# Kernel optimization log

Hardware: AMD Instinct MI355X
Metric: run time of the kernel (lower is better)

The kernel has to match this reference:

```python
import jax, jax.numpy as jnp
import numpy as np

B, T, C, H, W = 2, 8, 4, 128, 128
P = 8; D = 128; DEPTH = 2; E = 4; HD = 2 * D
Hp, Wp = H // P, W // P; F2 = 2 * D; CPP = C * P * P


def _ln(x, g, b):
    m = x.mean(-1, keepdims=True)
    v = ((x - m) ** 2).mean(-1, keepdims=True)
    return (x - m) * jax.lax.rsqrt(v + 1e-5) * g + b


def setup_inputs():
    key = jax.random.key(0)
    it = iter(jax.random.split(key, 32))
    def n(shape, s=0.02):
        return jax.random.normal(next(it), shape, jnp.float32) * s
    z = lambda shape: jnp.zeros(shape, jnp.float32)
    return {
        "x": jax.random.normal(next(it), (B, T, C, H, W), jnp.float32),
        "dt": jax.random.uniform(next(it), (T,), jnp.float32, 0.1, 1.0),
        "enc_Wre": n((CPP, D)), "enc_Wim": n((CPP, D)),
        "dec_W": n((F2, CPP)), "dec_b": z((CPP,)),
        "ln_sp_g": jnp.ones((DEPTH, F2), jnp.float32), "ln_sp_b": z((DEPTH, F2)),
        "conv_W": n((DEPTH, F2, F2, 3, 3), 0.05), "conv_b": z((DEPTH, F2)),
        "E_re": n((DEPTH, D, D), 0.05), "E_im": n((DEPTH, D, D), 0.05),
        "Dc_re": n((DEPTH, D, D), 0.05), "Dc_im": n((DEPTH, D, D), 0.05),
        "gate_W": n((DEPTH, F2, D)), "gate_b": z((DEPTH, D)),
        "src_W": n((DEPTH, F2, F2)), "src_b": z((DEPTH, F2)),
        "flux_decay": z((DEPTH, D)),
        "lam_re": n((DEPTH, D), 0.5), "lam_im": n((DEPTH, D), 0.5),
        "ln_t_g": jnp.ones((DEPTH, F2), jnp.float32), "ln_t_b": z((DEPTH, F2)),
        "rtr_W": n((DEPTH, F2, E)),
        "W1": n((DEPTH, E, F2, HD)), "b1": z((DEPTH, E, HD)),
        "W2": n((DEPTH, E, HD, F2)), "b2": z((DEPTH, E, F2)),
    }


def _forward(x, dt, enc_Wre, enc_Wim, dec_W, dec_b, ln_sp_g, ln_sp_b, conv_W, conv_b,
             E_re, E_im, Dc_re, Dc_im, gate_W, gate_b, src_W, src_b, flux_decay,
             lam_re, lam_im, ln_t_g, ln_t_b, rtr_W, W1, b1, W2, b2):
    Bx, Tx = x.shape[:2]
    # patch-embed encoder -> complex latent [B,T,D,Hp,Wp]
    f = x.reshape(Bx, Tx, C, Hp, P, Wp, P).transpose(0, 1, 3, 5, 2, 4, 6).reshape(Bx, Tx, Hp, Wp, CPP)
    zc = (f @ enc_Wre) + 1j * (f @ enc_Wim)
    zc = zc.transpose(0, 1, 4, 2, 3)
    dtBT = jnp.broadcast_to(dt[None, :], (Bx, Tx))
    flux = jnp.zeros((Bx, D), jnp.complex64)
    for i in range(DEPTH):
        # spatial branch: LayerNorm over [re,im] channels + Clifford-style 3x3 conv
        zr = jnp.concatenate([zc.real, zc.imag], axis=2).reshape(Bx * Tx, F2, Hp, Wp)
        xn = _ln(zr.transpose(0, 2, 3, 1), ln_sp_g[i], ln_sp_b[i]).transpose(0, 3, 1, 2)
        xs = jax.lax.conv_general_dilated(xn, conv_W[i], (1, 1), 'SAME',
                                          dimension_numbers=('NCHW', 'OIHW', 'NCHW')) + conv_b[i][None, :, None, None]
        sre, sim = jnp.split(xs, 2, axis=1)
        zc = zc + (sre + 1j * sim).reshape(Bx, Tx, D, Hp, Wp)
        # eigen-basis encode (complex channel mixing)
        xe = zc.transpose(0, 1, 3, 4, 2) @ (E_re[i] + 1j * E_im[i])  # B,T,Hp,Wp,D
        xm = xe.mean(axis=(2, 3))  # B,T,D complex
        # sequential flux tracker: inherently recurrent -> lax.scan over T
        gW, gb, sW, sb = gate_W[i], gate_b[i], src_W[i], src_b[i]
        dec = jax.nn.sigmoid(flux_decay[i])
        def step(fl, xmt):
            inp = jnp.concatenate([xmt.real, xmt.imag], -1)
            gate = jax.nn.sigmoid(inp @ gW + gb)
            s2 = inp @ sW + sb
            src = s2[..., :D] + 1j * s2[..., D:]
            fn = dec * fl + gate * xmt + (1.0 - gate) * src
            return fn, (fn, src)
        flux, (flux_seq, src_seq) = jax.lax.scan(step, flux, xm.transpose(1, 0, 2))
        flux_seq = flux_seq.transpose(1, 0, 2)
        src_seq = src_seq.transpose(1, 0, 2)
        g = jax.nn.sigmoid(jnp.concatenate([flux_seq.real, flux_seq.imag], -1) @ gW + gb)[:, :, None, None, :]
        forcing = xe * g + src_seq[:, :, None, None, :] * (1.0 - g)
        # complex transition operators (ZOH-style discretization)
        lam = -jax.nn.softplus(lam_re[i]) + 1j * lam_im[i]  # [D]
        opd = jnp.exp(dtBT[:, :, None] * lam[None, None, :])  # B,T,D complex
        opf = (opd - 1.0) / lam
        u = forcing * opf[:, :, None, None, :]
        A = jnp.broadcast_to(opd[:, :, None, None, :], u.shape)
        def comb(a, b):
            aA, aX = a
            bA, bX = b
            return (aA * bA, bX + bA * aX)
        # parallel pscan over time: h_t = A_t*h_{t-1} + u_t, independent per (B,Hp,Wp)
        _, uo = jax.lax.associative_scan(comb, (A, u), axis=1)
        xo = uo @ (Dc_re[i] + 1j * Dc_im[i])  # basis decode, B,T,Hp,Wp,D
        xon = _ln(jnp.concatenate([xo.real, xo.imag], -1), ln_t_g[i], ln_t_b[i])
        xcc = xon[..., :D] + 1j * xon[..., D:]
        # MoE FFN with soft routing over experts
        ft = jnp.concatenate([xcc.real, xcc.imag], -1).reshape(-1, F2)  # [M,2D]
        gates = jax.nn.softmax(ft @ rtr_W[i], axis=-1)  # [M,E]
        hmid = jax.nn.gelu(jnp.einsum('mf,efh->emh', ft, W1[i]) + b1[i][:, None, :])
        oexp = jnp.einsum('emh,ehf->emf', hmid, W2[i]) + b2[i][:, None, :]
        dtok = jnp.einsum('me,emf->mf', gates, oexp).reshape(Bx, Tx, Hp, Wp, F2)
        delta = dtok[..., :D] + 1j * dtok[..., D:]
        zc = zc + (xcc + delta).transpose(0, 1, 4, 2, 3)
    # decoder: project [re,im] -> pixels and unpatchify (real output)
    zl = zc.transpose(0, 1, 3, 4, 2)
    fo = jnp.concatenate([zl.real, zl.imag], -1) @ dec_W + dec_b
    return fo.reshape(Bx, Tx, Hp, Wp, C, P, P).transpose(0, 1, 4, 2, 5, 3, 6).reshape(Bx, Tx, C, H, W)


def reference(x, dt, enc_Wre, enc_Wim, dec_W, dec_b, ln_sp_g, ln_sp_b, conv_W, conv_b,
              E_re, E_im, Dc_re, Dc_im, gate_W, gate_b, src_W, src_b, flux_decay,
              lam_re, lam_im, ln_t_g, ln_t_b, rtr_W, W1, b1, W2, b2):
    return _forward(x, dt, enc_Wre, enc_Wim, dec_W, dec_b, ln_sp_g, ln_sp_b, conv_W, conv_b,
                    E_re, E_im, Dc_re, Dc_im, gate_W, gate_b, src_W, src_b, flux_decay,
                    lam_re, lam_im, ln_t_g, ln_t_b, rtr_W, W1, b1, W2, b2)
```

## Files before the change

kernel.cpp:

```cpp
#include <hip/hip_runtime.h>
#include <hip/hip_bf16.h>
#include <math.h>


#define NIN 28
typedef unsigned short u16;
typedef __attribute__((ext_vector_type(8))) short bf16x8;
typedef __attribute__((ext_vector_type(4))) float f32x4;
typedef __attribute__((ext_vector_type(8))) unsigned short us8;
typedef __attribute__((ext_vector_type(4))) unsigned short us4;

__device__ __forceinline__ float b2f(u16 u){ union{unsigned i;float f;}v; v.i=((unsigned)u)<<16; return v.f; }
__device__ __forceinline__ u16 f2b(float x){ __hip_bfloat16 h=__float2bfloat16(x); return *(u16*)&h; }
__device__ __forceinline__ float loadraw(const void* p, size_t i, int bf){
  return bf? b2f(((const u16*)p)[i]) : ((const float*)p)[i];
}
__device__ __forceinline__ float d_sigmoid(float x){ return 1.0f/(1.0f+expf(-x)); }
__device__ __forceinline__ float d_softplus(float x){ return fmaxf(x,0.0f)+log1pf(expf(-fabsf(x))); }
__device__ __forceinline__ float d_gelu(float x){
  const float c=0.7978845608028654f;
  return 0.5f*x*(1.0f+tanhf(c*(x+0.044715f*x*x*x)));
}

__global__ void detect_k(const void* lnspg, int* flag){
  unsigned w=*(const unsigned*)lnspg;
  *flag=(w==0x3F803F80u)?1:0;
}

#define NF32 17
struct MP {
  const void* src[NIN];
  int f32dst[NF32]; int f32cum[NF32+1];
  int seg[7];
};

__global__ __launch_bounds__(256) void mega_prep(MP a, const int* __restrict__ flag, float* __restrict__ W,
    u16* __restrict__ encB, u16* __restrict__ decB, u16* __restrict__ convB,
    u16* __restrict__ cplxB, u16* __restrict__ w1B, u16* __restrict__ w2c){
  int g=blockIdx.x*256+threadIdx.x;
  if(g>=a.seg[6]) return;
  int bf=*flag;
  if(g<a.seg[0]){
    int i=0;
    while(i<NF32-1 && g>=a.f32cum[i+1]) i++;
    int local=g-a.f32cum[i];
    const int needs[NF32]={1,5,6,7,9,14,15,16,17,18,19,20,21,22,23,25,27};
    W[a.f32dst[i]+local]=loadraw(a.src[needs[i]], local, bf);
  } else if(g<a.seg[1]){
    int idx=g-a.seg[0]; int n=idx>>8, k=idx&255;
    float v=(n<128)? loadraw(a.src[2],(size_t)k*128+n,bf) : loadraw(a.src[3],(size_t)k*128+(n-128),bf);
    encB[idx]=f2b(v);
  } else if(g<a.seg[2]){
    int idx=g-a.seg[1]; int n=idx>>8, k=idx&255;
    decB[idx]=f2b(loadraw(a.src[4],(size_t)k*256+n,bf));
  } else if(g<a.seg[3]){
    int idx=g-a.seg[2];
    int i=idx/589824; int r=idx-i*589824;
    int o=r/2304; int k=r-o*2304;
    int kg=k>>8, ic=k&255; int ky=kg/3, kx=kg-3*ky;
    size_t s=((((size_t)i*256+o)*256+ic)*3+ky)*3+kx;
    convB[idx]=f2b(loadraw(a.src[8],s,bf));
  } else if(g<a.seg[4]){
    int idx=g-a.seg[3];
    int mat=idx>>16; int r=idx&65535; int n=r>>8, k=r&255;
    int depth=mat&1; int isD=mat>>1;
    const void* re=isD? a.src[12]:a.src[10];
    const void* im=isD? a.src[13]:a.src[11];
    size_t base=(size_t)depth*16384;
    float v;
    if(k<128){ v = (n<128)? loadraw(re,base+(size_t)k*128+n,bf) : loadraw(im,base+(size_t)k*128+(n-128),bf); }
    else{ int kk=k-128;
      v = (n<128)? -loadraw(im,base+(size_t)kk*128+n,bf) : loadraw(re,base+(size_t)kk*128+(n-128),bf); }
    cplxB[idx]=f2b(v);
  } else if(g<a.seg[5]){
    int idx=g-a.seg[4]; int m=idx>>16; int r=idx&65535; int n=r>>8, k=r&255;
    w1B[idx]=f2b(loadraw(a.src[24],(size_t)m*65536+(size_t)k*256+n,bf));
  } else {
    int idx=g-a.seg[5];
    int i=idx>>18; int r=idx&262143; int n=r>>10; int k=r&1023;
    int e=k>>8, h=k&255;
    size_t s=(((size_t)(i*4+e)*256+h)*256+n);
    w2c[idx]=f2b(loadraw(a.src[26],s,bf));
  }
}

#define FB_BIAS 1
#define FB_GELU 2
#define FB_RS 4
#define FB_ADDTO 8
#define FB_WF32 16
#define FB_WBF16 32
#define FB_CONV 64
#define FB_GATHER 128
#define FB_MOE2 256
#define FB_UNPATCH 512
#define FB_XM 1024

template<int FLAGS>
__global__ __launch_bounds__(256,4) void mfma_gemm(
    const void* __restrict__ Asrc, const u16* __restrict__ Bt,
    const float* __restrict__ bias, const float* __restrict__ gates,
    float* __restrict__ Cf, u16* __restrict__ Cb,
    const u16* __restrict__ Xtra, void* __restrict__ Cout, const int* __restrict__ flagp,
    int K, long aE, long bE, long biasE, long cE, long cRow,
    float* __restrict__ xm4)
{
  __shared__ u16 As[2][64][72];
  __shared__ u16 Bs[2][64][72];
  const int e=blockIdx.z;
  const u16* A=(const u16*)Asrc + (size_t)e*aE;
  Bt += (size_t)e*bE;
  const float* biasp = bias? bias+(size_t)e*biasE : nullptr;
  const int bn=blockIdx.x*64, bm=blockIdx.y*64;
  const int tid=threadIdx.x, l=tid&63, w=tid>>6;
  const int wm=w&1, wn=w>>1;
  int bf=0;
  if(FLAGS&(FB_GATHER|FB_UNPATCH)) bf=*flagp;
  const us8 z8={0,0,0,0,0,0,0,0};

  auto loadAi=[&](int k0, int i)->us8{
    int c=tid+(i<<8); int row=c>>3, col8=(c&7)<<3;
    int gk=k0+col8;
    if(FLAGS&FB_CONV){
      int m=bm+row; int bt=m>>8, rem=m&255, hp=rem>>4, wp=rem&15;
      int kg=gk>>8, ic=gk&255; int ky=kg/3, kx=kg-3*ky;
      int y=hp+ky-1, x=wp+kx-1;
      return ((unsigned)y<16u && (unsigned)x<16u)?
           *(const us8*)&A[(((size_t)(bt*16+y))*16+x)*256+ic] : z8;
    } else if(FLAGS&FB_GATHER){
      int m=bm+row; int bt=m>>8, rem=m&255, hp=rem>>4, wp=rem&15;
      int c2=gk>>6, ph=(gk>>3)&7;
      size_t sidx=(((size_t)bt*4+c2)<<14)+(size_t)((hp*8+ph)<<7)+wp*8;
      if(bf) return *(const us8*)&((const u16*)Asrc)[sidx];
      const float* xf=(const float*)Asrc + sidx;
      us8 t;
      #pragma unroll
      for(int j=0;j<8;j++) t[j]=f2b(xf[j]);
      return t;
    }
    return *(const us8*)&A[(size_t)(bm+row)*K+gk];
  };
  auto loadBi=[&](int k0, int i)->us8{
    int c=tid+(i<<8); int row=c>>3, col8=(c&7)<<3;
    return *(const us8*)&Bt[(size_t)(bn+row)*K+k0+col8];
  };

  us8 ra0,ra1,rb0,rb1;
  ra0=loadAi(0,0); ra1=loadAi(0,1); rb0=loadBi(0,0); rb1=loadBi(0,1);
  {
    int c0=tid, c1=tid+256;
    *(us8*)&As[0][c0>>3][(c0&7)<<3]=ra0;
    *(us8*)&As[0][c1>>3][(c1&7)<<3]=ra1;
    *(us8*)&Bs[0][c0>>3][(c0&7)<<3]=rb0;
    *(us8*)&Bs[0][c1>>3][(c1&7)<<3]=rb1;
  }
  const int kSteps=K>>6;
  if(kSteps>1){ ra0=loadAi(64,0); ra1=loadAi(64,1); rb0=loadBi(64,0); rb1=loadBi(64,1); }
  __syncthreads();

  f32x4 zf={0.f,0.f,0.f,0.f};
  f32x4 acc00=zf, acc01=zf, acc10=zf, acc11=zf;

  const int aRow0=wm*32+(l&15), bRow0=wn*32+(l&15);
  const int kcL=(l>>4)<<3;

  for(int ks=0; ks<kSteps; ++ks){
    const int cur=ks&1;
    if(ks+1<kSteps){
      int nb=cur^1;
      int c0=tid, c1=tid+256;
      *(us8*)&As[nb][c0>>3][(c0&7)<<3]=ra0;
      *(us8*)&As[nb][c1>>3][(c1&7)<<3]=ra1;
      *(us8*)&Bs[nb][c0>>3][(c0&7)<<3]=rb0;
      *(us8*)&Bs[nb][c1>>3][(c1&7)<<3]=rb1;
      if(ks+2<kSteps){
        int k0=(ks+2)<<6;
        ra0=loadAi(k0,0); ra1=loadAi(k0,1); rb0=loadBi(k0,0); rb1=loadBi(k0,1);
      }
    }
    #pragma unroll
    for(int kk=0;kk<64;kk+=32){
      const int kc=kk+kcL;
      bf16x8 a0=*(const bf16x8*)&As[cur][aRow0   ][kc];
      bf16x8 a1=*(const bf16x8*)&As[cur][aRow0+16][kc];
      bf16x8 b0=*(const bf16x8*)&Bs[cur][bRow0   ][kc];
      bf16x8 b1=*(const bf16x8*)&Bs[cur][bRow0+16][kc];
      acc00=__builtin_amdgcn_mfma_f32_16x16x32_bf16(a0,b0,acc00,0,0,0);
      acc01=__builtin_amdgcn_mfma_f32_16x16x32_bf16(a0,b1,acc01,0,0,0);
      acc10=__builtin_amdgcn_mfma_f32_16x16x32_bf16(a1,b0,acc10,0,0,0);
      acc11=__builtin_amdgcn_mfma_f32_16x16x32_bf16(a1,b1,acc11,0,0,0);
    }
    __syncthreads();
  }

  const int rr=(l>>4)<<2, cc=l&15;
  #pragma unroll
  for(int mi=0;mi<2;mi++){
    #pragma unroll
    for(int ni=0;ni<2;ni++){
      f32x4 av = mi? (ni?acc11:acc10) : (ni?acc01:acc00);
      #pragma unroll
      for(int r=0;r<4;r++){
        int m=bm+wm*32+mi*16+rr+r;
        int n=bn+wn*32+ni*16+cc;
        float v=av[r];
        if(FLAGS&FB_BIAS) v+=biasp[n];
        if(FLAGS&FB_GELU) v=d_gelu(v);
        if(FLAGS&FB_RS)   v*=gates[(size_t)m*4+e];
        if(FLAGS&FB_MOE2){
          #pragma unroll
          for(int ee=0;ee<4;ee++) v+=gates[(size_t)m*4+ee]*bias[ee*256+n];
          v+=b2f(Xtra[(size_t)m*256+n]);
        }
        if(FLAGS&FB_UNPATCH){
          int bt=m>>8, hp=(m>>4)&15, wp=m&15;
          int c=n>>6, ph=(n>>3)&7, pw=n&7;
          size_t o=((size_t)bt<<16)|((size_t)c<<14)|((size_t)(hp*8+ph)<<7)|(size_t)(wp*8+pw);
          if(bf) ((__hip_bfloat16*)Cout)[o]=__float2bfloat16(v);
          else   ((float*)Cout)[o]=v;
          continue;
        }
        size_t o=(size_t)e*cE + (size_t)m*cRow + n;
        if(FLAGS&FB_ADDTO) v+=Cf[o];
        if(FLAGS&(FB_WF32|FB_ADDTO)) Cf[o]=v;
        if(FLAGS&FB_WBF16) Cb[o]=f2b(v);
      }
    }
  }

  if(FLAGS&FB_XM){
    float cs0=acc00[0]+acc00[1]+acc00[2]+acc00[3] + acc10[0]+acc10[1]+acc10[2]+acc10[3];
    float cs1=acc01[0]+acc01[1]+acc01[2]+acc01[3] + acc11[0]+acc11[1]+acc11[2]+acc11[3];
    cs0+=__shfl_xor(cs0,16); cs0+=__shfl_xor(cs0,32);
    cs1+=__shfl_xor(cs1,16); cs1+=__shfl_xor(cs1,32);
    float* xr=(float*)&As[0][0][0];
    if(l<16){
      xr[wm*64 + wn*32 + cc]      = cs0;
      xr[wm*64 + wn*32 + 16 + cc] = cs1;
    }
    __syncthreads();
    if(tid<64){
      float s=xr[tid]+xr[64+tid];
      xm4[(size_t)blockIdx.y*256 + bn + tid]=s;
    }
  }
}

__global__ __launch_bounds__(256) void ln4_k(const float* __restrict__ X,
    const float* __restrict__ g, const float* __restrict__ b, u16* __restrict__ out,
    const float* __restrict__ rtr, float* __restrict__ gates){
  int row=blockIdx.x*4+(threadIdx.x>>6);
  int l=threadIdx.x&63;
  f32x4 v=*(const f32x4*)&X[(size_t)row*256+l*4];
  float s=v[0]+v[1]+v[2]+v[3];
  #pragma unroll
  for(int o=32;o;o>>=1) s+=__shfl_xor(s,o);
  float mean=s*(1.0f/256.0f);
  float d0=v[0]-mean,d1=v[1]-mean,d2=v[2]-mean,d3=v[3]-mean;
  float q=d0*d0+d1*d1+d2*d2+d3*d3;
  #pragma unroll
  for(int o=32;o;o>>=1) q+=__shfl_xor(q,o);
  float rs=rsqrtf(q*(1.0f/256.0f)+1e-5f);
  float nv[4]={d0,d1,d2,d3};
  us4 o4;
  #pragma unroll
  for(int j=0;j<4;j++){ nv[j]=nv[j]*rs*g[l*4+j]+b[l*4+j]; o4[j]=f2b(nv[j]); }
  *(us4*)&out[(size_t)row*256+l*4]=o4;
  if(rtr){
    float p[4]={0.f,0.f,0.f,0.f};
    #pragma unroll
    for(int j=0;j<4;j++)
      #pragma unroll
      for(int ee=0;ee<4;ee++) p[ee]+=nv[j]*rtr[(l*4+j)*4+ee];
    #pragma unroll
    for(int ee=0;ee<4;ee++)
      #pragma unroll
      for(int o=32;o;o>>=1) p[ee]+=__shfl_xor(p[ee],o);
    if(l==0){
      float mx=fmaxf(fmaxf(p[0],p[1]),fmaxf(p[2],p[3]));
      float e0=expf(p[0]-mx),e1=expf(p[1]-mx),e2=expf(p[2]-mx),e3=expf(p[3]-mx);
      float inv=1.0f/(e0+e1+e2+e3);
      gates[row*4+0]=e0*inv; gates[row*4+1]=e1*inv; gates[row*4+2]=e2*inv; gates[row*4+3]=e3*inv;
    }
  }
}

__global__ __launch_bounds__(384) void gate_src_k(const float* __restrict__ xm4,
    const float* __restrict__ sW, const float* __restrict__ sb,
    const float* __restrict__ gW, const float* __restrict__ gb,
    float* __restrict__ xm, float* __restrict__ s2, float* __restrict__ gt,
    const float* __restrict__ dt, const float* __restrict__ lam_re, const float* __restrict__ lam_im,
    float* __restrict__ odr_, float* __restrict__ odi_, float* __restrict__ ofr_, float* __restrict__ ofi_){
  int tid=threadIdx.x;
  if(blockIdx.x==16){
    for(int idx=tid; idx<1024; idx+=384){
      int t=idx>>7, d=idx&127;
      float lr=-d_softplus(lam_re[d]);
      float li=lam_im[d];
      float dtv=dt[t];
      float er=expf(dtv*lr);
      float odr=er*cosf(dtv*li), odi=er*sinf(dtv*li);
      float den=lr*lr+li*li;
      float ar=odr-1.0f, ai=odi;
      odr_[idx]=odr; odi_[idx]=odi;
      ofr_[idx]=(ar*lr+ai*li)/den;
      ofi_[idx]=(ai*lr-ar*li)/den;
    }
    return;
  }
  int bt=blockIdx.x;
  __shared__ float inp[256];
  if(tid<256){
    int rb=bt*4;
    float v=(xm4[(size_t)rb*256+tid]+xm4[(size_t)(rb+1)*256+tid]
            +xm4[(size_t)(rb+2)*256+tid]+xm4[(size_t)(rb+3)*256+tid])*(1.0f/256.0f);
    inp[tid]=v; xm[bt*256+tid]=v;
  }
  __syncthreads();
  if(tid<256){
    float acc=sb[tid];
    #pragma unroll 8
    for(int k=0;k<256;k++) acc+=inp[k]*sW[k*256+tid];
    s2[bt*256+tid]=acc;
  }else{
    int d=tid-256;
    float acc=gb[d];
    #pragma unroll 8
    for(int k=0;k<256;k++) acc+=inp[k]*gW[k*128+d];
    gt[bt*128+d]=d_sigmoid(acc);
  }
}

__global__ __launch_bounds__(128) void flux_gate2(const float* __restrict__ xm,
    const float* __restrict__ s2, const float* __restrict__ gt,
    const float* __restrict__ fdec, const float* __restrict__ fbin, float* __restrict__ fbout,
    const float* __restrict__ gW, const float* __restrict__ gb, float* __restrict__ gbuf, int init){
  int bt=blockIdx.x; int b=bt>>3, t=bt&7; int d=threadIdx.x;
  float flr = init? 0.f : fbin[b*256+d];
  float fli = init? 0.f : fbin[b*256+128+d];
  float dec = d_sigmoid(fdec[d]);
  for(int tp=0; tp<=t; tp++){
    int q=b*8+tp;
    float gv=gt[q*128+d];
    flr = dec*flr + gv*xm[q*256+d]     + (1.0f-gv)*s2[q*256+d];
    fli = dec*fli + gv*xm[q*256+128+d] + (1.0f-gv)*s2[q*256+128+d];
  }
  __shared__ float inp[256];
  inp[d]=flr; inp[128+d]=fli;
  __syncthreads();
  float acc=gb[d];
  #pragma unroll 8
  for(int k=0;k<256;k++) acc+=inp[k]*gW[k*128+d];
  gbuf[bt*128+d]=d_sigmoid(acc);
  if(t==7){ fbout[b*256+d]=flr; fbout[b*256+128+d]=fli; }
}

__global__ __launch_bounds__(256) void fscan_t(const float* __restrict__ xe,
    const float* __restrict__ gbuf, const float* __restrict__ ss,
    const float* __restrict__ odr, const float* __restrict__ odi,
    const float* __restrict__ ofr, const float* __restrict__ ofi, u16* __restrict__ uo){
  int idx=blockIdx.x*256+threadIdx.x;
  int d=idx&127, s=(idx>>7)&255, b=idx>>15;
  float hr=0.f, hi=0.f;
  for(int t=0;t<8;t++){
    int bt=b*8+t;
    size_t n=(size_t)bt*256+s;
    float g=gbuf[bt*128+d];
    float sr=ss[bt*256+d], si=ss[bt*256+128+d];
    float xr=xe[n*256+d], xi=xe[n*256+128+d];
    float fr=xr*g+sr*(1.0f-g), fi=xi*g+si*(1.0f-g);
    float pr=ofr[t*128+d], pi=ofi[t*128+d];
    float ur=fr*pr-fi*pi, ui=fr*pi+fi*pr;
    float ar=odr[t*128+d], ai=odi[t*128+d];
    float nr=ar*hr-ai*hi+ur, ni=ar*hi+ai*hr+ui;
    hr=nr; hi=ni;
    uo[n*256+d]=f2b(hr); uo[n*256+128+d]=f2b(hi);
  }
}

extern "C" void kernel_launch(void* const* d_in, const int* in_sizes, int n_in,
                              void* d_out, int out_size, void* d_ws, size_t ws_size,
                              hipStream_t stream){
  (void)out_size; (void)ws_size; (void)n_in;
  int acum[NIN+1]; acum[0]=0;
  for(int i=0;i<NIN;i++) acum[i+1]=acum[i]+((i==0)?0:in_sizes[i]);
  const int totalA=acum[NIN];
  float* W=(float*)d_ws;
  size_t off=((size_t)totalA+63)&~(size_t)63;
  int*   flag=(int*)(W+off); off+=64;
  float* zc  =W+off; off+=1048576;
  float* xe  =W+off; off+=1048576;
  u16* zcb =(u16*)(W+off); off+=524288;
  u16* xnb =(u16*)(W+off); off+=524288;
  u16* uob =(u16*)(W+off); off+=524288;
  u16* ftb =(u16*)(W+off); off+=524288;
  u16* hmid=(u16*)(W+off); off+=2097152;
  u16* encB=(u16*)(W+off); off+=32768;
  u16* decB=(u16*)(W+off); off+=32768;
  u16* convB=(u16*)(W+off); off+=589824;
  u16* cplxB=(u16*)(W+off); off+=131072;
  u16* w1B =(u16*)(W+off); off+=262144;
  u16* w2c =(u16*)(W+off); off+=262144;
  float* xm4 =W+off; off+=16384;
  float* xm  =W+off; off+=4096;
  float* s2  =W+off; off+=4096;
  float* gt  =W+off; off+=2048;
  float* gbuf=W+off; off+=2048;
  float* odr =W+off; off+=1024;
  float* odi =W+off; off+=1024;
  float* ofr =W+off; off+=1024;
  float* ofi =W+off; off+=1024;
  float* gates=W+off; off+=16384;
  float* fbA =W+off; off+=512;
  float* fbB =W+off; off+=512;

  detect_k<<<1,1,0,stream>>>(d_in[6], flag);

  MP mp;
  for(int i=0;i<NIN;i++) mp.src[i]=d_in[i];
  const int needs[NF32]={1,5,6,7,9,14,15,16,17,18,19,20,21,22,23,25,27};
  mp.f32cum[0]=0;
  for(int j=0;j<NF32;j++){ mp.f32cum[j+1]=mp.f32cum[j]+in_sizes[needs[j]]; mp.f32dst[j]=acum[needs[j]]; }
  mp.seg[0]=mp.f32cum[NF32];
  mp.seg[1]=mp.seg[0]+65536;
  mp.seg[2]=mp.seg[1]+65536;
  mp.seg[3]=mp.seg[2]+1179648;
  mp.seg[4]=mp.seg[3]+262144;
  mp.seg[5]=mp.seg[4]+524288;
  mp.seg[6]=mp.seg[5]+524288;
  mega_prep<<<(mp.seg[6]+255)/256,256,0,stream>>>(mp, flag, W, encB, decB, convB, cplxB, w1B, w2c);

  const dim3 GG(4,64,1);
  mfma_gemm<FB_GATHER|FB_WF32><<<GG,256,0,stream>>>(d_in[0], encB, nullptr, nullptr,
      zc, nullptr, nullptr, nullptr, flag, 256, 0,0,0,0,256, nullptr);

  for(int i=0;i<2;i++){
    const float* lnspg=W+acum[6]+i*256;
    const float* lnspb=W+acum[7]+i*256;
    const float* convb=W+acum[9]+i*256;
    const float* gWp  =W+acum[14]+i*32768;
    const float* gbp  =W+acum[15]+i*128;
    const float* sWp  =W+acum[16]+i*65536;
    const float* sbp  =W+acum[17]+i*256;
    const float* fdec =W+acum[18]+i*128;
    const float* lamre=W+acum[19]+i*128;
    const float* lamim=W+acum[20]+i*128;
    const float* lntg =W+acum[21]+i*256;
    const float* lntb =W+acum[22]+i*256;
    const float* rtr  =W+acum[23]+i*1024;
    const float* b1   =W+acum[25]+i*1024;
    const float* b2   =W+acum[27]+i*1024;

    ln4_k<<<1024,256,0,stream>>>(zc, lnspg, lnspb, xnb, nullptr, nullptr);
    mfma_gemm<FB_CONV|FB_BIAS|FB_ADDTO|FB_WBF16><<<GG,256,0,stream>>>(xnb, convB+(size_t)i*589824,
        convb, nullptr, zc, zcb, nullptr, nullptr, nullptr, 2304, 0,0,0,0,256, nullptr);
    mfma_gemm<FB_WF32|FB_XM><<<GG,256,0,stream>>>(zcb, cplxB+(size_t)i*65536, nullptr, nullptr,
        xe, nullptr, nullptr, nullptr, nullptr, 256, 0,0,0,0,256, xm4);
    gate_src_k<<<17,384,0,stream>>>(xm4, sWp, sbp, gWp, gbp, xm, s2, gt,
        W+acum[1], lamre, lamim, odr, odi, ofr, ofi);
    flux_gate2<<<16,128,0,stream>>>(xm, s2, gt, fdec, (i==0)?nullptr:fbA, (i==0)?fbA:fbB,
        gWp, gbp, gbuf, (i==0)?1:0);
    fscan_t<<<256,256,0,stream>>>(xe, gbuf, s2, odr, odi, ofr, ofi, uob);
    mfma_gemm<FB_WF32><<<GG,256,0,stream>>>(uob, cplxB+(size_t)(2+i)*65536, nullptr, nullptr,
        xe, nullptr, nullptr, nullptr, nullptr, 256, 0,0,0,0,256, nullptr);
    ln4_k<<<1024,256,0,stream>>>(xe, lntg, lntb, ftb, rtr, gates);
    mfma_gemm<FB_BIAS|FB_GELU|FB_RS|FB_WBF16><<<dim3(4,64,4),256,0,stream>>>(ftb, w1B+(size_t)i*262144,
        b1, gates, nullptr, hmid, nullptr, nullptr, nullptr, 256, 0,65536,256,256,1024, nullptr);
    mfma_gemm<FB_MOE2|FB_ADDTO|FB_WBF16><<<GG,256,0,stream>>>(hmid, w2c+(size_t)i*262144,
        b2, gates, zc, zcb, ftb, nullptr, nullptr, 1024, 0,0,0,0,256, nullptr);
  }

  mfma_gemm<FB_BIAS|FB_UNPATCH><<<GG,256,0,stream>>>(zcb, decB, W+acum[5], nullptr,
      nullptr, nullptr, nullptr, d_out, flag, 256, 0,0,0,0,256, nullptr);
}
```

Measured before the change: 212.2 us.

## Fuse LayerNorm and router into full-row GEMM epilogues and drop detect kernel

Adds a full-row GEMM kernel (16 rows × 256 cols per block) whose epilogue computes LayerNorm and, optionally, the router softmax. This removes the separate ln4_k launches after the encoder, the decoder-of-state GEMM and the first-depth MoE down-projection. The bf16-detect kernel is replaced by an inline check inside each kernel. The conv weight repack now goes through a per-output-channel LDS transpose to get coalesced reads. In exchange, the fused GEMMs launch only 256 blocks and reload the whole B matrix per block, and variance is now computed as E[x²]−mean², which is less numerically stable.

Result: faster. 191.8 us (-9.6%).

```diff
diff --git a/kernel.cpp b/kernel.cpp
--- a/kernel.cpp
+++ b/kernel.cpp
@@ -8,13 +8,13 @@
 typedef __attribute__((ext_vector_type(8))) short bf16x8;
 typedef __attribute__((ext_vector_type(4))) float f32x4;
 typedef __attribute__((ext_vector_type(8))) unsigned short us8;
-typedef __attribute__((ext_vector_type(4))) unsigned short us4;
 
 __device__ __forceinline__ float b2f(u16 u){ union{unsigned i;float f;}v; v.i=((unsigned)u)<<16; return v.f; }
 __device__ __forceinline__ u16 f2b(float x){ __hip_bfloat16 h=__float2bfloat16(x); return *(u16*)&h; }
 __device__ __forceinline__ float loadraw(const void* p, size_t i, int bf){
   return bf? b2f(((const u16*)p)[i]) : ((const float*)p)[i];
 }
+__device__ __forceinline__ int bfflag(const void* p){ return *(const unsigned*)p==0x3F803F80u; }
 __device__ __forceinline__ float d_sigmoid(float x){ return 1.0f/(1.0f+expf(-x)); }
 __device__ __forceinline__ float d_softplus(float x){ return fmaxf(x,0.0f)+log1pf(expf(-fabsf(x))); }
 __device__ __forceinline__ float d_gelu(float x){
@@ -22,24 +22,32 @@
   return 0.5f*x*(1.0f+tanhf(c*(x+0.044715f*x*x*x)));
 }
 
-__global__ void detect_k(const void* lnspg, int* flag){
-  unsigned w=*(const unsigned*)lnspg;
-  *flag=(w==0x3F803F80u)?1:0;
-}
-
 #define NF32 17
 struct MP {
   const void* src[NIN];
   int f32dst[NF32]; int f32cum[NF32+1];
-  int seg[7];
+  int seg[6];
 };
 
-__global__ __launch_bounds__(256) void mega_prep(MP a, const int* __restrict__ flag, float* __restrict__ W,
+__global__ __launch_bounds__(256) void mega_prep(MP a, float* __restrict__ W,
     u16* __restrict__ encB, u16* __restrict__ decB, u16* __restrict__ convB,
     u16* __restrict__ cplxB, u16* __restrict__ w1B, u16* __restrict__ w2c){
-  int g=blockIdx.x*256+threadIdx.x;
-  if(g>=a.seg[6]) return;
-  int bf=*flag;
+  const int bf=bfflag(a.src[6]);
+  const int tid=threadIdx.x;
+  if(blockIdx.x<512){
+    __shared__ float lds[2304];
+    int io=blockIdx.x;
+    size_t base=(size_t)io*2304;
+    for(int r=tid;r<2304;r+=256) lds[r]=loadraw(a.src[8], base+r, bf);
+    __syncthreads();
+    for(int k=tid;k<2304;k+=256){
+      int ic=k&255, kg=k>>8;
+      convB[base+k]=f2b(lds[ic*9+kg]);
+    }
+    return;
+  }
+  int g=(blockIdx.x-512)*256+tid;
+  if(g>=a.seg[5]) return;
   if(g<a.seg[0]){
     int i=0;
     while(i<NF32-1 && g>=a.f32cum[i+1]) i++;
@@ -55,13 +63,6 @@
     decB[idx]=f2b(loadraw(a.src[4],(size_t)k*256+n,bf));
   } else if(g<a.seg[3]){
     int idx=g-a.seg[2];
-    int i=idx/589824; int r=idx-i*589824;
-    int o=r/2304; int k=r-o*2304;
-    int kg=k>>8, ic=k&255; int ky=kg/3, kx=kg-3*ky;
-    size_t s=((((size_t)i*256+o)*256+ic)*3+ky)*3+kx;
-    convB[idx]=f2b(loadraw(a.src[8],s,bf));
-  } else if(g<a.seg[4]){
-    int idx=g-a.seg[3];
     int mat=idx>>16; int r=idx&65535; int n=r>>8, k=r&255;
     int depth=mat&1; int isD=mat>>1;
     const void* re=isD? a.src[12]:a.src[10];
@@ -72,11 +73,11 @@
     else{ int kk=k-128;
       v = (n<128)? -loadraw(im,base+(size_t)kk*128+n,bf) : loadraw(re,base+(size_t)kk*128+(n-128),bf); }
     cplxB[idx]=f2b(v);
-  } else if(g<a.seg[5]){
-    int idx=g-a.seg[4]; int m=idx>>16; int r=idx&65535; int n=r>>8, k=r&255;
+  } else if(g<a.seg[4]){
+    int idx=g-a.seg[3]; int m=idx>>16; int r=idx&65535; int n=r>>8, k=r&255;
     w1B[idx]=f2b(loadraw(a.src[24],(size_t)m*65536+(size_t)k*256+n,bf));
   } else {
-    int idx=g-a.seg[5];
+    int idx=g-a.seg[4];
     int i=idx>>18; int r=idx&262143; int n=r>>10; int k=r&1023;
     int e=k>>8, h=k&255;
     size_t s=(((size_t)(i*4+e)*256+h)*256+n);
@@ -91,7 +92,6 @@
 #define FB_WF32 16
 #define FB_WBF16 32
 #define FB_CONV 64
-#define FB_GATHER 128
 #define FB_MOE2 256
 #define FB_UNPATCH 512
 #define FB_XM 1024
@@ -101,7 +101,7 @@
     const void* __restrict__ Asrc, const u16* __restrict__ Bt,
     const float* __restrict__ bias, const float* __restrict__ gates,
     float* __restrict__ Cf, u16* __restrict__ Cb,
-    const u16* __restrict__ Xtra, void* __restrict__ Cout, const int* __restrict__ flagp,
+    const u16* __restrict__ Xtra, void* __restrict__ Cout, const void* __restrict__ flagp,
     int K, long aE, long bE, long biasE, long cE, long cRow,
     float* __restrict__ xm4)
 {
@@ -115,7 +115,7 @@
   const int tid=threadIdx.x, l=tid&63, w=tid>>6;
   const int wm=w&1, wn=w>>1;
   int bf=0;
-  if(FLAGS&(FB_GATHER|FB_UNPATCH)) bf=*flagp;
+  if(FLAGS&FB_UNPATCH) bf=bfflag(flagp);
   const us8 z8={0,0,0,0,0,0,0,0};
 
   auto loadAi=[&](int k0, int i)->us8{
@@ -127,16 +127,6 @@
       int y=hp+ky-1, x=wp+kx-1;
       return ((unsigned)y<16u && (unsigned)x<16u)?
            *(const us8*)&A[(((size_t)(bt*16+y))*16+x)*256+ic] : z8;
-    } else if(FLAGS&FB_GATHER){
-      int m=bm+row; int bt=m>>8, rem=m&255, hp=rem>>4, wp=rem&15;
-      int c2=gk>>6, ph=(gk>>3)&7;
-      size_t sidx=(((size_t)bt*4+c2)<<14)+(size_t)((hp*8+ph)<<7)+wp*8;
-      if(bf) return *(const us8*)&((const u16*)Asrc)[sidx];
-      const float* xf=(const float*)Asrc + sidx;
-      us8 t;
-      #pragma unroll
-      for(int j=0;j<8;j++) t[j]=f2b(xf[j]);
-      return t;
     }
     return *(const us8*)&A[(size_t)(bm+row)*K+gk];
   };
@@ -160,7 +150,6 @@
 
   f32x4 zf={0.f,0.f,0.f,0.f};
   f32x4 acc00=zf, acc01=zf, acc10=zf, acc11=zf;
-
   const int aRow0=wm*32+(l&15), bRow0=wn*32+(l&15);
   const int kcL=(l>>4)<<3;
 
@@ -246,41 +235,194 @@
   }
 }
 
-__global__ __launch_bounds__(256) void ln4_k(const float* __restrict__ X,
-    const float* __restrict__ g, const float* __restrict__ b, u16* __restrict__ out,
-    const float* __restrict__ rtr, float* __restrict__ gates){
-  int row=blockIdx.x*4+(threadIdx.x>>6);
-  int l=threadIdx.x&63;
-  f32x4 v=*(const f32x4*)&X[(size_t)row*256+l*4];
-  float s=v[0]+v[1]+v[2]+v[3];
+#define FR_GATHER 1
+#define FR_WF32 2
+#define FR_MOE2 4
+#define FR_ADDTO 8
+#define FR_LN 16
+#define FR_RTR 32
+
+template<int FLAGS>
+__global__ __launch_bounds__(256) void gemm_fullrow(
+    const void* __restrict__ Asrc, const u16* __restrict__ Bt,
+    const float* __restrict__ b2, const float* __restrict__ gatesIn,
+    float* __restrict__ Cf, const u16* __restrict__ Xtra,
+    const float* __restrict__ lnG, const float* __restrict__ lnB, u16* __restrict__ lnOut,
+    const float* __restrict__ rtr, float* __restrict__ gatesOut,
+    const void* __restrict__ flagp, int K)
+{
+  __shared__ u16 As[2][16][72];
+  __shared__ u16 Bs[2][256][72];
+  __shared__ float sc[480];
+  const int bm=blockIdx.x*16;
+  const int tid=threadIdx.x, l=tid&63, w=tid>>6;
+  int bf=0;
+  if(FLAGS&FR_GATHER) bf=bfflag(flagp);
+  const bool aAct = tid<128;
+
+  auto loadA=[&](int k0)->us8{
+    int row=tid>>3, col8=(tid&7)<<3;
+    int gk=k0+col8;
+    if(FLAGS&FR_GATHER){
+      int m=bm+row; int bt=m>>8, rem=m&255, hp=rem>>4, wp=rem&15;
+      int c2=gk>>6, ph=(gk>>3)&7;
+      size_t sidx=(((size_t)bt*4+c2)<<14)+(size_t)((hp*8+ph)<<7)+wp*8;
+      if(bf) return *(const us8*)&((const u16*)Asrc)[sidx];
+      const float* xf=(const float*)Asrc+sidx;
+      us8 t;
+      #pragma unroll
+      for(int j=0;j<8;j++) t[j]=f2b(xf[j]);
+      return t;
+    }
+    return *(const us8*)&((const u16*)Asrc)[(size_t)(bm+row)*K+gk];
+  };
+  auto loadB=[&](int k0, int j)->us8{
+    int c=tid+(j<<8); int row=c>>3, col8=(c&7)<<3;
+    return *(const us8*)&Bt[(size_t)row*K+k0+col8];
+  };
+
+  us8 ra, rb[8];
+  if(aAct) ra=loadA(0);
   #pragma unroll
-  for(int o=32;o;o>>=1) s+=__shfl_xor(s,o);
-  float mean=s*(1.0f/256.0f);
-  float d0=v[0]-mean,d1=v[1]-mean,d2=v[2]-mean,d3=v[3]-mean;
-  float q=d0*d0+d1*d1+d2*d2+d3*d3;
+  for(int j=0;j<8;j++) rb[j]=loadB(0,j);
+  if(aAct) *(us8*)&As[0][tid>>3][(tid&7)<<3]=ra;
   #pragma unroll
-  for(int o=32;o;o>>=1) q+=__shfl_xor(q,o);
-  float rs=rsqrtf(q*(1.0f/256.0f)+1e-5f);
-  float nv[4]={d0,d1,d2,d3};
-  us4 o4;
+  for(int j=0;j<8;j++){ int c=tid+(j<<8); *(us8*)&Bs[0][c>>3][(c&7)<<3]=rb[j]; }
+  const int kSteps=K>>6;
+  if(kSteps>1){ if(aAct) ra=loadA(64); 
+    #pragma unroll
+    for(int j=0;j<8;j++) rb[j]=loadB(64,j); }
+  __syncthreads();
+
+  f32x4 zf={0.f,0.f,0.f,0.f};
+  f32x4 acc[4]={zf,zf,zf,zf};
+  const int kcL=(l>>4)<<3;
+
+  for(int ks=0; ks<kSteps; ++ks){
+    const int cur=ks&1;
+    if(ks+1<kSteps){
+      int nb=cur^1;
+      if(aAct) *(us8*)&As[nb][tid>>3][(tid&7)<<3]=ra;
+      #pragma unroll
+      for(int j=0;j<8;j++){ int c=tid+(j<<8); *(us8*)&Bs[nb][c>>3][(c&7)<<3]=rb[j]; }
+      if(ks+2<kSteps){
+        int k0=(ks+2)<<6;
+        if(aAct) ra=loadA(k0);
+        #pragma unroll
+        for(int j=0;j<8;j++) rb[j]=loadB(k0,j);
+      }
+    }
+    #pragma unroll
+    for(int kk=0;kk<64;kk+=32){
+      const int kc=kk+kcL;
+      bf16x8 a=*(const bf16x8*)&As[cur][l&15][kc];
+      #pragma unroll
+      for(int ni=0;ni<4;ni++){
+        bf16x8 b=*(const bf16x8*)&Bs[cur][w*64+ni*16+(l&15)][kc];
+        acc[ni]=__builtin_amdgcn_mfma_f32_16x16x32_bf16(a,b,acc[ni],0,0,0);
+      }
+    }
+    __syncthreads();
+  }
+
+  const int rr=(l>>4)<<2, cc=l&15;
+  float v[4][4];
   #pragma unroll
-  for(int j=0;j<4;j++){ nv[j]=nv[j]*rs*g[l*4+j]+b[l*4+j]; o4[j]=f2b(nv[j]); }
-  *(us4*)&out[(size_t)row*256+l*4]=o4;
-  if(rtr){
-    float p[4]={0.f,0.f,0.f,0.f};
-    #pragma unroll
-    for(int j=0;j<4;j++)
-      #pragma unroll
-      for(int ee=0;ee<4;ee++) p[ee]+=nv[j]*rtr[(l*4+j)*4+ee];
-    #pragma unroll
-    for(int ee=0;ee<4;ee++)
-      #pragma unroll
-      for(int o=32;o;o>>=1) p[ee]+=__shfl_xor(p[ee],o);
-    if(l==0){
-      float mx=fmaxf(fmaxf(p[0],p[1]),fmaxf(p[2],p[3]));
-      float e0=expf(p[0]-mx),e1=expf(p[1]-mx),e2=expf(p[2]-mx),e3=expf(p[3]-mx);
-      float inv=1.0f/(e0+e1+e2+e3);
-      gates[row*4+0]=e0*inv; gates[row*4+1]=e1*inv; gates[row*4+2]=e2*inv; gates[row*4+3]=e3*inv;
+  for(int ni=0;ni<4;ni++){
+    #pragma unroll
+    for(int r=0;r<4;r++){
+      int m=bm+rr+r, n=w*64+ni*16+cc;
+      float x=acc[ni][r];
+      if(FLAGS&FR_MOE2){
+        #pragma unroll
+        for(int ee=0;ee<4;ee++) x+=gatesIn[(size_t)m*4+ee]*b2[ee*256+n];
+        x+=b2f(Xtra[(size_t)m*256+n]);
+      }
+      size_t o=(size_t)m*256+n;
+      if(FLAGS&FR_ADDTO) x+=Cf[o];
+      if(FLAGS&(FR_WF32|FR_ADDTO)) Cf[o]=x;
+      v[ni][r]=x;
+    }
+  }
+
+  if(FLAGS&FR_LN){
+    float rs[4]={0,0,0,0}, rq[4]={0,0,0,0};
+    #pragma unroll
+    for(int ni=0;ni<4;ni++)
+      #pragma unroll
+      for(int r=0;r<4;r++){ rs[r]+=v[ni][r]; rq[r]+=v[ni][r]*v[ni][r]; }
+    #pragma unroll
+    for(int o=1;o<16;o<<=1){
+      #pragma unroll
+      for(int r=0;r<4;r++){ rs[r]+=__shfl_xor(rs[r],o); rq[r]+=__shfl_xor(rq[r],o); }
+    }
+    if((l&15)==0){
+      int q=l>>4;
+      #pragma unroll
+      for(int r=0;r<4;r++){ sc[w*16+q*4+r]=rs[r]; sc[64+w*16+q*4+r]=rq[r]; }
+    }
+    __syncthreads();
+    if(tid<16){
+      float tot=0,tq=0;
+      #pragma unroll
+      for(int w4=0;w4<4;w4++){ tot+=sc[w4*16+tid]; tq+=sc[64+w4*16+tid]; }
+      float mean=tot*(1.0f/256.0f);
+      float var=tq*(1.0f/256.0f)-mean*mean;
+      sc[128+tid]=mean; sc[144+tid]=rsqrtf(var+1e-5f);
+    }
+    __syncthreads();
+    float nvv[4][4];
+    #pragma unroll
+    for(int ni=0;ni<4;ni++)
+      #pragma unroll
+      for(int r=0;r<4;r++){
+        int row=rr+r, n=w*64+ni*16+cc;
+        float nv=(v[ni][r]-sc[128+row])*sc[144+row]*lnG[n]+lnB[n];
+        nvv[ni][r]=nv;
+        lnOut[(size_t)(bm+row)*256+n]=f2b(nv);
+      }
+    if(FLAGS&FR_RTR){
+      float pe[4][4]={{0,0,0,0},{0,0,0,0},{0,0,0,0},{0,0,0,0}};
+      #pragma unroll
+      for(int ni=0;ni<4;ni++){
+        int n=w*64+ni*16+cc;
+        #pragma unroll
+        for(int r=0;r<4;r++)
+          #pragma unroll
+          for(int e=0;e<4;e++) pe[r][e]+=nvv[ni][r]*rtr[n*4+e];
+      }
+      #pragma unroll
+      for(int o=1;o<16;o<<=1)
+        #pragma unroll
+        for(int r=0;r<4;r++)
+          #pragma unroll
+          for(int e=0;e<4;e++) pe[r][e]+=__shfl_xor(pe[r][e],o);
+      if((l&15)==0){
+        int q=l>>4;
+        #pragma unroll
+        for(int r=0;r<4;r++)
+          #pragma unroll
+          for(int e=0;e<4;e++) sc[160+w*64+(q*4+r)*4+e]=pe[r][e];
+      }
+      __syncthreads();
+      if(tid<64){
+        int row=tid>>2, e=tid&3;
+        float t=0;
+        #pragma unroll
+        for(int w4=0;w4<4;w4++) t+=sc[160+w4*64+row*4+e];
+        sc[416+row*4+e]=t;
+      }
+      __syncthreads();
+      if(tid<16){
+        float a0=sc[416+tid*4],a1=sc[416+tid*4+1],a2=sc[416+tid*4+2],a3=sc[416+tid*4+3];
+        float mx=fmaxf(fmaxf(a0,a1),fmaxf(a2,a3));
+        float e0=expf(a0-mx),e1=expf(a1-mx),e2=expf(a2-mx),e3=expf(a3-mx);
+        float inv=1.0f/(e0+e1+e2+e3);
+        gatesOut[(size_t)(bm+tid)*4+0]=e0*inv;
+        gatesOut[(size_t)(bm+tid)*4+1]=e1*inv;
+        gatesOut[(size_t)(bm+tid)*4+2]=e2*inv;
+        gatesOut[(size_t)(bm+tid)*4+3]=e3*inv;
+      }
     }
   }
 }
@@ -387,7 +529,6 @@
   const int totalA=acum[NIN];
   float* W=(float*)d_ws;
   size_t off=((size_t)totalA+63)&~(size_t)63;
-  int*   flag=(int*)(W+off); off+=64;
   float* zc  =W+off; off+=1048576;
   float* xe  =W+off; off+=1048576;
   u16* zcb =(u16*)(W+off); off+=524288;
@@ -414,8 +555,6 @@
   float* fbA =W+off; off+=512;
   float* fbB =W+off; off+=512;
 
-  detect_k<<<1,1,0,stream>>>(d_in[6], flag);
-
   MP mp;
   for(int i=0;i<NIN;i++) mp.src[i]=d_in[i];
   const int needs[NF32]={1,5,6,7,9,14,15,16,17,18,19,20,21,22,23,25,27};
@@ -424,19 +563,20 @@
   mp.seg[0]=mp.f32cum[NF32];
   mp.seg[1]=mp.seg[0]+65536;
   mp.seg[2]=mp.seg[1]+65536;
-  mp.seg[3]=mp.seg[2]+1179648;
-  mp.seg[4]=mp.seg[3]+262144;
+  mp.seg[3]=mp.seg[2]+262144;
+  mp.seg[4]=mp.seg[3]+524288;
   mp.seg[5]=mp.seg[4]+524288;
-  mp.seg[6]=mp.seg[5]+524288;
-  mega_prep<<<(mp.seg[6]+255)/256,256,0,stream>>>(mp, flag, W, encB, decB, convB, cplxB, w1B, w2c);
+  int restBlocks=(mp.seg[5]+255)/256;
+  mega_prep<<<512+restBlocks,256,0,stream>>>(mp, W, encB, decB, convB, cplxB, w1B, w2c);
 
   const dim3 GG(4,64,1);
-  mfma_gemm<FB_GATHER|FB_WF32><<<GG,256,0,stream>>>(d_in[0], encB, nullptr, nullptr,
-      zc, nullptr, nullptr, nullptr, flag, 256, 0,0,0,0,256, nullptr);
+  const float* lnspg0=W+acum[6];
+
+  gemm_fullrow<FR_GATHER|FR_WF32|FR_LN><<<256,256,0,stream>>>(d_in[0], encB,
+      nullptr, nullptr, zc, nullptr,
+      W+acum[6]+0*256, W+acum[7]+0*256, xnb, nullptr, nullptr, d_in[6], 256);
 
   for(int i=0;i<2;i++){
-    const float* lnspg=W+acum[6]+i*256;
-    const float* lnspb=W+acum[7]+i*256;
     const float* convb=W+acum[9]+i*256;
     const float* gWp  =W+acum[14]+i*32768;
     const float* gbp  =W+acum[15]+i*128;
@@ -451,7 +591,6 @@
     const float* b1   =W+acum[25]+i*1024;
     const float* b2   =W+acum[27]+i*1024;
 
-    ln4_k<<<1024,256,0,stream>>>(zc, lnspg, lnspb, xnb, nullptr, nullptr);
     mfma_gemm<FB_CONV|FB_BIAS|FB_ADDTO|FB_WBF16><<<GG,256,0,stream>>>(xnb, convB+(size_t)i*589824,
         convb, nullptr, zc, zcb, nullptr, nullptr, nullptr, 2304, 0,0,0,0,256, nullptr);
     mfma_gemm<FB_WF32|FB_XM><<<GG,256,0,stream>>>(zcb, cplxB+(size_t)i*65536, nullptr, nullptr,
@@ -461,15 +600,21 @@
     flux_gate2<<<16,128,0,stream>>>(xm, s2, gt, fdec, (i==0)?nullptr:fbA, (i==0)?fbA:fbB,
         gWp, gbp, gbuf, (i==0)?1:0);
     fscan_t<<<256,256,0,stream>>>(xe, gbuf, s2, odr, odi, ofr, ofi, uob);
-    mfma_gemm<FB_WF32><<<GG,256,0,stream>>>(uob, cplxB+(size_t)(2+i)*65536, nullptr, nullptr,
-        xe, nullptr, nullptr, nullptr, nullptr, 256, 0,0,0,0,256, nullptr);
-    ln4_k<<<1024,256,0,stream>>>(xe, lntg, lntb, ftb, rtr, gates);
+    gemm_fullrow<FR_LN|FR_RTR><<<256,256,0,stream>>>(uob, cplxB+(size_t)(2+i)*65536,
+        nullptr, nullptr, nullptr, nullptr,
+        lntg, lntb, ftb, rtr, gates, nullptr, 256);
     mfma_gemm<FB_BIAS|FB_GELU|FB_RS|FB_WBF16><<<dim3(4,64,4),256,0,stream>>>(ftb, w1B+(size_t)i*262144,
         b1, gates, nullptr, hmid, nullptr, nullptr, nullptr, 256, 0,65536,256,256,1024, nullptr);
-    mfma_gemm<FB_MOE2|FB_ADDTO|FB_WBF16><<<GG,256,0,stream>>>(hmid, w2c+(size_t)i*262144,
-        b2, gates, zc, zcb, ftb, nullptr, nullptr, 1024, 0,0,0,0,256, nullptr);
+    if(i==0){
+      gemm_fullrow<FR_MOE2|FR_ADDTO|FR_WF32|FR_LN><<<256,256,0,stream>>>(hmid, w2c,
+          b2, gates, zc, ftb,
+          W+acum[6]+1*256, W+acum[7]+1*256, xnb, nullptr, nullptr, nullptr, 1024);
+    }else{
+      mfma_gemm<FB_MOE2|FB_ADDTO|FB_WBF16><<<GG,256,0,stream>>>(hmid, w2c+262144,
+          b2, gates, zc, zcb, ftb, nullptr, nullptr, 1024, 0,0,0,0,256, nullptr);
+    }
   }
 
   mfma_gemm<FB_BIAS|FB_UNPATCH><<<GG,256,0,stream>>>(zcb, decB, W+acum[5], nullptr,
-      nullptr, nullptr, nullptr, d_out, flag, 256, 0,0,0,0,256, nullptr);
-}
+      nullptr, nullptr, nullptr, d_out, d_in[6], 256, 0,0,0,0,256, nullptr);
+}
```
